# Kernel optimization log

Hardware: AMD Instinct MI355X
Metric: run time of the kernel (lower is better)

## Reference

```python
import jax, jax.numpy as jnp
import numpy as np


def conv2d(x, w, b, stride, pad):
    # x: NCHW, w: OIHW (torch layout)
    y = jax.lax.conv_general_dilated(
        x, w, (stride, stride), ((pad, pad), (pad, pad)),
        dimension_numbers=('NCHW', 'OIHW', 'NCHW'))
    return y + b[None, :, None, None]


def conv_transpose2d(x, w, b, stride, pad):
    # w: torch ConvTranspose2d layout [in, out, kH, kW]
    k = w.shape[2]
    w_t = jnp.flip(w, (2, 3)).transpose(1, 0, 2, 3)  # -> OIHW
    p = k - 1 - pad
    y = jax.lax.conv_general_dilated(
        x, w_t, (1, 1), ((p, p), (p, p)), lhs_dilation=(stride, stride),
        dimension_numbers=('NCHW', 'OIHW', 'NCHW'))
    return y + b[None, :, None, None]


def resblock(x, w1, b1, w2, b2):
    h = jax.nn.relu(x)
    h = conv2d(h, w1, b1, 1, 1)   # 3x3
    h = jax.nn.relu(h)
    h = conv2d(h, w2, b2, 1, 0)   # 1x1
    return x + h


def setup_inputs() -> dict:
    key = jax.random.key(0)
    ks = iter(jax.random.split(key, 32))
    K, D = 512, 256
    s = 0.05

    def rn(shape):
        return (jax.random.normal(next(ks), shape, dtype=jnp.float32) * s)

    inp = {
        'x': jax.random.uniform(next(ks), (32, 3, 128, 128), dtype=jnp.float32),
        'e_c1_w': rn((256, 3, 4, 4)),   'e_c1_b': jnp.zeros((256,), jnp.float32),
        'e_c2_w': rn((256, 256, 4, 4)), 'e_c2_b': jnp.zeros((256,), jnp.float32),
        'e_r1_w1': rn((256, 256, 3, 3)), 'e_r1_b1': jnp.zeros((256,), jnp.float32),
        'e_r1_w2': rn((256, 256, 1, 1)), 'e_r1_b2': jnp.zeros((256,), jnp.float32),
        'e_r2_w1': rn((256, 256, 3, 3)), 'e_r2_b1': jnp.zeros((256,), jnp.float32),
        'e_r2_w2': rn((256, 256, 1, 1)), 'e_r2_b2': jnp.zeros((256,), jnp.float32),
        'emb': jax.random.normal(next(ks), (K, D), dtype=jnp.float32) / K,
        'd_r1_w1': rn((256, 256, 3, 3)), 'd_r1_b1': jnp.zeros((256,), jnp.float32),
        'd_r1_w2': rn((256, 256, 1, 1)), 'd_r1_b2': jnp.zeros((256,), jnp.float32),
        'd_r2_w1': rn((256, 256, 3, 3)), 'd_r2_b1': jnp.zeros((256,), jnp.float32),
        'd_r2_w2': rn((256, 256, 1, 1)), 'd_r2_b2': jnp.zeros((256,), jnp.float32),
        'd_t1_w': rn((256, 256, 4, 4)), 'd_t1_b': jnp.zeros((256,), jnp.float32),
        'd_t2_w': rn((256, 3, 4, 4)),   'd_t2_b': jnp.zeros((3,), jnp.float32),
    }
    return inp


def reference(x, e_c1_w, e_c1_b, e_c2_w, e_c2_b,
              e_r1_w1, e_r1_b1, e_r1_w2, e_r1_b2,
              e_r2_w1, e_r2_b1, e_r2_w2, e_r2_b2,
              emb,
              d_r1_w1, d_r1_b1, d_r1_w2, d_r1_b2,
              d_r2_w1, d_r2_b1, d_r2_w2, d_r2_b2,
              d_t1_w, d_t1_b, d_t2_w, d_t2_b):
    # ---- encoder ----
    h = jax.nn.relu(conv2d(x, e_c1_w, e_c1_b, 2, 1))
    h = jax.nn.relu(conv2d(h, e_c2_w, e_c2_b, 2, 1))
    h = resblock(h, e_r1_w1, e_r1_b1, e_r1_w2, e_r1_b2)
    z_e_x = resblock(h, e_r2_w1, e_r2_b1, e_r2_w2, e_r2_b2)  # [B,256,h,w]

    # ---- VQ: fused squared-distance + argmin (same math as
    # sum((z - e)^2, -2).argmin(-1), without the (B,h,w,256,K) intermediate) ----
    z = z_e_x.transpose(0, 2, 3, 1)                      # [B,h,w,256]
    z2 = jnp.sum(z * z, axis=-1, keepdims=True)          # [B,h,w,1]
    e2 = jnp.sum(emb * emb, axis=-1)                     # [K]
    dists = z2 - 2.0 * jnp.einsum('bhwd,kd->bhwk', z, emb) + e2
    latents = jnp.argmin(dists, axis=-1)                 # [B,h,w] int

    # ---- decoder ----
    z_q = emb[latents]                                   # [B,h,w,256]
    z_q_x = z_q.transpose(0, 3, 1, 2)                    # [B,256,h,w]
    d = resblock(z_q_x, d_r1_w1, d_r1_b1, d_r1_w2, d_r1_b2)
    d = resblock(d, d_r2_w1, d_r2_b1, d_r2_w2, d_r2_b2)
    d = jax.nn.relu(conv_transpose2d(d, d_t1_w, d_t1_b, 2, 1))
    x_tilde = jax.nn.sigmoid(conv_transpose2d(d, d_t2_w, d_t2_b, 2, 1))
    return x_tilde, z_e_x, z_q_x
```

## Files before the change

### kernel.cpp

```cpp
#include <hip/hip_runtime.h>
#include <math.h>

using frag_ab = __attribute__((ext_vector_type(8))) short;
using f32x4   = __attribute__((ext_vector_type(4))) float;

__device__ __forceinline__ unsigned short f2b(float f) {
    unsigned u = __float_as_uint(f);
    u += 0x7fffu + ((u >> 16) & 1u);
    return (unsigned short)(u >> 16);
}
__device__ __forceinline__ void bf8_to_f(uint4 v, float* f) {
    const unsigned* p = (const unsigned*)&v;
    #pragma unroll
    for (int q = 0; q < 4; ++q) {
        unsigned u = p[q];
        f[2*q]   = __uint_as_float(u << 16);
        f[2*q+1] = __uint_as_float(u & 0xffff0000u);
    }
}
__device__ __forceinline__ void gload16(const void* g, void* l) {
    __builtin_amdgcn_global_load_lds(g, l, 16, 0, 0);
}

__global__ void k_wt(const float* __restrict__ in, unsigned short* __restrict__ out,
                     int total, int CO, int CI, int sO, int sI) {
    int i = blockIdx.x * 256 + threadIdx.x;
    if (i >= total) return;
    int ci = i % CI;
    int r  = i / CI;
    int co = r % CO;
    int tp = r / CO;
    out[i] = f2b(in[(size_t)co * sO + (size_t)ci * sI + tp]);
}
__global__ void k_wt16(const float* __restrict__ in, unsigned short* __restrict__ out,
                       int sO, int sI) {
    int i = blockIdx.x * 256 + threadIdx.x;
    int ci = i & 255, co = i >> 8;
    const float* p = in + (size_t)co * sO + (size_t)ci * sI;
    #pragma unroll
    for (int tp = 0; tp < 16; ++tp)
        out[tp * 65536 + i] = f2b(p[tp]);
}
__global__ void k_wt3(const float* p0, const float* p1, const float* p2, const float* p3,
                      unsigned short* o0, unsigned short* o1, unsigned short* o2,
                      unsigned short* o3) {
    int z = blockIdx.y;
    const float* in = (z == 0) ? p0 : (z == 1) ? p1 : (z == 2) ? p2 : p3;
    unsigned short* out = (z == 0) ? o0 : (z == 1) ? o1 : (z == 2) ? o2 : o3;
    int i = blockIdx.x * 256 + threadIdx.x;
    int ci = i & 255, co = i >> 8;
    const float* p = in + (size_t)co * 2304 + (size_t)ci * 9;
    #pragma unroll
    for (int tp = 0; tp < 9; ++tp)
        out[tp * 65536 + i] = f2b(p[tp]);
}
__global__ void k_wt1(const float* p0, const float* p1, const float* p2, const float* p3,
                      unsigned short* o0, unsigned short* o1, unsigned short* o2,
                      unsigned short* o3) {
    int z = blockIdx.y;
    const float* in = (z == 0) ? p0 : (z == 1) ? p1 : (z == 2) ? p2 : p3;
    unsigned short* out = (z == 0) ? o0 : (z == 1) ? o1 : (z == 2) ? o2 : o3;
    int i = blockIdx.x * 256 + threadIdx.x;
    int ci = i & 255, co = i >> 8;
    out[i] = f2b(in[co * 256 + ci]);
}
__global__ void k_embcast(const float* __restrict__ in, unsigned short* __restrict__ out) {
    int i = blockIdx.x * 256 + threadIdx.x;
    out[i] = f2b(in[i]);
}

__global__ void k_e2(const float* __restrict__ emb, float* __restrict__ e2,
                     float* __restrict__ zpad) {
    if (blockIdx.x == 2) { zpad[threadIdx.x] = 0.f; return; }
    int k = blockIdx.x * 256 + threadIdx.x;
    if (k < 512) {
        const float* r = emb + k * 256;
        float s = 0.f;
        #pragma unroll 8
        for (int d = 0; d < 256; ++d) s += r[d] * r[d];
        e2[k] = s;
    }
}

__global__ __launch_bounds__(256) void k_conv1(const float* __restrict__ x,
        const float* __restrict__ w, const float* __restrict__ bias,
        unsigned short* __restrict__ out) {
    int t = threadIdx.x;
    int y = blockIdx.x * 4 + (t >> 6);
    int xq = t & 63;
    int b = blockIdx.y;
    int co0 = blockIdx.z * 64;
    float patch[48];
    #pragma unroll
    for (int ci = 0; ci < 3; ++ci)
        #pragma unroll
        for (int ky = 0; ky < 4; ++ky)
            #pragma unroll
            for (int kx = 0; kx < 4; ++kx) {
                int sy = 2*y - 1 + ky, sx = 2*xq - 1 + kx;
                float v = 0.f;
                if ((unsigned)sy < 128u && (unsigned)sx < 128u)
                    v = x[((b*3 + ci)*128 + sy)*128 + sx];
                patch[(ci*4 + ky)*4 + kx] = v;
            }
    unsigned short* op = out + (((size_t)(b*64 + y)*64 + xq) << 8) + co0;
    for (int c8 = 0; c8 < 8; ++c8) {
        unsigned short u8[8];
        #pragma unroll
        for (int cc = 0; cc < 8; ++cc) {
            int co = co0 + c8*8 + cc;
            float a = bias[co];
            #pragma unroll
            for (int k = 0; k < 48; ++k) a = fmaf(w[co*48 + k], patch[k], a);
            u8[cc] = f2b(fmaxf(a, 0.f));
        }
        *(uint4*)(op + c8*8) = *(uint4*)u8;
    }
}

template<int MODE, bool RELU_OUT, bool RELU_B16>
__global__ __launch_bounds__(256) void k_cgemm(
        const unsigned short* __restrict__ A,
        const unsigned short* __restrict__ Wt,
        const float* __restrict__ bias,
        const float* __restrict__ skipF,
        const unsigned short* __restrict__ zpad,
        unsigned short* __restrict__ outB,
        float* __restrict__ outFn,
        float* __restrict__ outFc) {
    constexpr int NTAPS = (MODE==0) ? 16 : (MODE==1) ? 9 : (MODE==2) ? 1 : 4;
    constexpr int NCH   = NTAPS * 4;
    constexpr int HIN   = (MODE==0) ? 64 : 32;
    constexpr bool ISCT = (MODE==3);

    __shared__ __align__(16) unsigned short As[2][128*64];
    __shared__ __align__(16) unsigned short Bs[2][128*64];

    int t = threadIdx.x;
    int cob = blockIdx.x;
    int y0  = blockIdx.y * 4;
    int bz  = blockIdx.z;
    int b   = ISCT ? (bz >> 2) : bz;
    int par = ISCT ? (bz & 3) : 0;
    int psy = par >> 1, psx = par & 1;

    int srow = t >> 3;
    int scc  = t & 7;
    int sc2  = scc ^ (srow & 7);

    int wv = t >> 6, lane = t & 63;
    int mq = (wv >> 1) * 64, nq = (wv & 1) * 64;
    int lg = lane >> 4, lr = lane & 15;

    f32x4 acc[4][4];
    #pragma unroll
    for (int i = 0; i < 4; ++i)
        #pragma unroll
        for (int j = 0; j < 4; ++j) acc[i][j] = (f32x4){0.f,0.f,0.f,0.f};

    auto stage = [&](int n, int buf) {
        int tap = n >> 2, kk0 = (n & 3) * 64;
        int tdy, tdx, wtap;
        if (MODE == 0)      { tdy = tap >> 2; tdx = tap & 3; wtap = tap; }
        else if (MODE == 1) { tdy = tap / 3;  tdx = tap % 3; wtap = tap; }
        else if (MODE == 2) { tdy = 0; tdx = 0; wtap = 0; }
        else { int jy = tap >> 1, jx = tap & 1;
               tdy = psy - jy; tdx = psx - jx;
               wtap = ((psy ? 0 : 1) + 2*jy) * 4 + ((psx ? 0 : 1) + 2*jx); }
        const unsigned short* wb = Wt + ((size_t)wtap << 16) + ((size_t)cob << 15);
        #pragma unroll
        for (int q = 0; q < 4; ++q) {
            int row = srow + 32*q;
            int soy = y0 + (row >> 5), sox = row & 31;
            int sy = (MODE == 0) ? (2*soy - 1 + tdy)
                   : (MODE == 1) ? (soy - 1 + tdy) : (soy + tdy);
            int sx = (MODE == 0) ? (2*sox - 1 + tdx)
                   : (MODE == 1) ? (sox - 1 + tdx) : (sox + tdx);
            bool val = ((unsigned)sy < (unsigned)HIN) && ((unsigned)sx < (unsigned)HIN);
            const unsigned short* asrc = val
                ? A + ((((size_t)(b*HIN + sy))*HIN + sx) << 8) + kk0 + sc2*8
                : zpad;
            gload16(asrc, (char*)As[buf] + q*4096 + t*16);
            gload16(wb + (((size_t)row) << 8) + kk0 + sc2*8,
                    (char*)Bs[buf] + q*4096 + t*16);
        }
    };

    stage(0, 0);
    __syncthreads();
    for (int n = 0; n < NCH; ++n) {
        int cur = n & 1;
        if (n + 1 < NCH) stage(n + 1, cur ^ 1);
        #pragma unroll
        for (int ks = 0; ks < 2; ++ks) {
            int c = ks*4 + lg;
            frag_ab af[4], bf[4];
            #pragma unroll
            for (int i = 0; i < 4; ++i) {
                int ar = mq + i*16 + lr;
                af[i] = *(const frag_ab*)((const char*)As[cur] + ar*128 + ((c ^ (ar & 7)) << 4));
                int br = nq + i*16 + lr;
                bf[i] = *(const frag_ab*)((const char*)Bs[cur] + br*128 + ((c ^ (br & 7)) << 4));
            }
            #pragma unroll
            for (int i = 0; i < 4; ++i)
                #pragma unroll
                for (int j = 0; j < 4; ++j)
                    acc[i][j] = __builtin_amdgcn_mfma_f32_16x16x32_bf16(
                                    af[i], bf[j], acc[i][j], 0, 0, 0);
        }
        __syncthreads();
    }

    #pragma unroll
    for (int mf = 0; mf < 4; ++mf) {
        #pragma unroll
        for (int nf = 0; nf < 4; ++nf) {
            int co = cob*128 + nq + nf*16 + lr;
            float bb = bias[co];
            f32x4 v = acc[mf][nf];
            #pragma unroll
            for (int j = 0; j < 4; ++j) {
                int prow = mq + mf*16 + lg*4 + j;
                int oy = y0 + (prow >> 5);
                int ox = prow & 31;
                size_t pix;
                if (ISCT) pix = ((size_t)(b*64 + (2*oy + psy)))*64 + (2*ox + psx);
                else      pix = ((size_t)(b*32 + oy))*32 + ox;
                float xv = v[j] + bb;
                if (skipF) xv += skipF[pix*256 + co];
                if (RELU_OUT) xv = fmaxf(xv, 0.f);
                if (outB)  outB[pix*256 + co] = f2b(RELU_B16 ? fmaxf(xv, 0.f) : xv);
                if (outFn) outFn[pix*256 + co] = xv;
                if (outFc) outFc[(((size_t)b*256 + co) << 10) + oy*32 + ox] = xv;
            }
        }
    }
}

__global__ __launch_bounds__(256) void k_vqm(const unsigned short* __restrict__ zB,
        const unsigned short* __restrict__ eB,
        const float* __restrict__ e2, int* __restrict__ lat) {
    __shared__ __align__(16) unsigned short As[64*256];
    __shared__ __align__(16) unsigned short Bs[64*256];
    int t = threadIdx.x;
    int pos0 = blockIdx.x * 64;
    #pragma unroll
    for (int q = 0; q < 8; ++q) {
        int idx = q*256 + t;
        int row = idx >> 5, ch = idx & 31;
        uint4 v = *(const uint4*)(zB + (((size_t)(pos0 + row)) << 8) + ch*8);
        *(uint4*)((char*)As + row*512 + ((ch ^ (row & 7)) << 4)) = v;
    }
    int wv = t >> 6, lane = t & 63;
    int lg = lane >> 4, lr = lane & 15;
    int arow = wv*16 + lr;
    int aswz[8];
    #pragma unroll
    for (int kk = 0; kk < 8; ++kk)
        aswz[kk] = arow*512 + (((kk*4 + lg) ^ (arow & 7)) << 4);
    float minv[4] = {1e30f, 1e30f, 1e30f, 1e30f};
    int   mink[4] = {0, 0, 0, 0};
    for (int kc = 0; kc < 8; ++kc) {
        __syncthreads();
        #pragma unroll
        for (int q = 0; q < 8; ++q) {
            int idx = q*256 + t;
            int row = idx >> 5, ch = idx & 31;
            uint4 v = *(const uint4*)(eB + (((size_t)(kc*64 + row)) << 8) + ch*8);
            *(uint4*)((char*)Bs + row*512 + ((ch ^ (row & 7)) << 4)) = v;
        }
        __syncthreads();
        #pragma unroll
        for (int nt = 0; nt < 4; ++nt) {
            int brow = nt*16 + lr;
            f32x4 acc = (f32x4){0.f, 0.f, 0.f, 0.f};
            #pragma unroll
            for (int kk = 0; kk < 8; ++kk) {
                frag_ab a = *(const frag_ab*)((const char*)As + aswz[kk]);
                frag_ab b = *(const frag_ab*)((const char*)Bs
                              + brow*512 + (((kk*4 + lg) ^ (brow & 7)) << 4));
                acc = __builtin_amdgcn_mfma_f32_16x16x32_bf16(a, b, acc, 0, 0, 0);
            }
            int k = kc*64 + nt*16 + lr;
            float ee = e2[k];
            #pragma unroll
            for (int j = 0; j < 4; ++j) {
                float dist = ee - 2.f * acc[j];
                if (dist < minv[j]) { minv[j] = dist; mink[j] = k; }
            }
        }
    }
    #pragma unroll
    for (int s = 1; s < 16; s <<= 1) {
        #pragma unroll
        for (int j = 0; j < 4; ++j) {
            float ov = __shfl_xor(minv[j], s, 64);
            int   ok = __shfl_xor(mink[j], s, 64);
            if (ov < minv[j] || (ov == minv[j] && ok < mink[j])) {
                minv[j] = ov; mink[j] = ok;
            }
        }
    }
    if (lr == 0) {
        #pragma unroll
        for (int j = 0; j < 4; ++j)
            lat[pos0 + wv*16 + lg*4 + j] = mink[j];
    }
}

__global__ __launch_bounds__(256) void k_gather(const int* __restrict__ lat,
        const float* __restrict__ emb, float* __restrict__ zqc,
        unsigned short* __restrict__ zqB, float* __restrict__ zqF) {
    __shared__ int ll[32];
    int t = threadIdx.x, y = blockIdx.x, b = blockIdx.y;
    if (t < 32) ll[t] = lat[(b * 32 + y) * 32 + t];
    __syncthreads();
    #pragma unroll
    for (int i = 0; i < 32; ++i) {
        int l = i * 256 + t;
        int d = l >> 5, xx = l & 31;
        zqc[(((size_t)b*256 + d) << 10) + y*32 + xx] = emb[ll[xx]*256 + d];
    }
    int xx = t & 31, dg = t >> 5;
    const float* e = emb + ll[xx]*256 + dg*32;
    size_t off = ((((size_t)(b*32 + y)*32 + xx)) << 8) + dg*32;
    #pragma unroll
    for (int q = 0; q < 8; ++q) {
        float4 v = *(const float4*)(e + q*4);
        *(float4*)(zqF + off + q*4) = v;
        uint2 pk;
        pk.x = (unsigned)f2b(fmaxf(v.x, 0.f)) | ((unsigned)f2b(fmaxf(v.y, 0.f)) << 16);
        pk.y = (unsigned)f2b(fmaxf(v.z, 0.f)) | ((unsigned)f2b(fmaxf(v.w, 0.f)) << 16);
        *(uint2*)(zqB + off + q*4) = pk;
    }
}

__global__ __launch_bounds__(256) void k_convt2(const unsigned short* __restrict__ in,
        const unsigned short* __restrict__ Wt,
        const float* __restrict__ bias, float* __restrict__ out) {
    __shared__ __align__(16) unsigned short slab[4*66*40];
    __shared__ __align__(16) unsigned short wl[16*3*32];
    int t = threadIdx.x;
    int b = blockIdx.y;
    int oy0 = blockIdx.x * 4;
    int u0 = oy0 >> 1;
    int oyl = t >> 7, ox = t & 127;
    int sy = oyl & 1, sx = ox & 1;
    int v = ox >> 1;
    float acc0[3] = {0.f,0.f,0.f}, acc1[3] = {0.f,0.f,0.f};
    for (int kc = 0; kc < 8; ++kc) {
        __syncthreads();
        for (int i = t; i < 4*66*4; i += 256) {
            int g = i & 3; int cidx = i >> 2;
            int cc = cidx % 66, ri = cidx / 66;
            int iy = u0 - 1 + ri, ix = cc - 1;
            uint4 v4 = {0,0,0,0};
            if ((unsigned)iy < 64u && (unsigned)ix < 64u)
                v4 = *(const uint4*)(in + (((size_t)(b*64 + iy)*64 + ix) << 8)
                                        + kc*32 + g*8);
            *(uint4*)(&slab[(ri*66 + cc)*40 + g*8]) = v4;
        }
        for (int i = t; i < 1536; i += 256)
            wl[i] = Wt[(i >> 5) * 256 + kc*32 + (i & 31)];
        __syncthreads();
        #pragma unroll
        for (int jy = 0; jy < 2; ++jy) {
            int duy = sy - jy;
            int riA = 1 + duy;
            #pragma unroll
            for (int jx = 0; jx < 2; ++jx) {
                int dvx = sx - jx;
                int cc = v + dvx + 1;
                int wtap = ((sy ? 0 : 1) + 2*jy)*4 + ((sx ? 0 : 1) + 2*jx);
                const unsigned short* sA = &slab[(riA*66 + cc)*40];
                const unsigned short* sB = sA + 66*40;
                const unsigned short* wp = &wl[wtap*96];
                #pragma unroll
                for (int c8 = 0; c8 < 4; ++c8) {
                    float fA[8], fB[8], w0[8], w1[8], w2[8];
                    bf8_to_f(*(const uint4*)(sA + c8*8), fA);
                    bf8_to_f(*(const uint4*)(sB + c8*8), fB);
                    bf8_to_f(*(const uint4*)(wp + c8*8), w0);
                    bf8_to_f(*(const uint4*)(wp + 32 + c8*8), w1);
                    bf8_to_f(*(const uint4*)(wp + 64 + c8*8), w2);
                    #pragma unroll
                    for (int q = 0; q < 8; ++q) {
                        acc0[0] = fmaf(fA[q], w0[q], acc0[0]);
                        acc0[1] = fmaf(fA[q], w1[q], acc0[1]);
                        acc0[2] = fmaf(fA[q], w2[q], acc0[2]);
                        acc1[0] = fmaf(fB[q], w0[q], acc1[0]);
                        acc1[1] = fmaf(fB[q], w1[q], acc1[1]);
                        acc1[2] = fmaf(fB[q], w2[q], acc1[2]);
                    }
                }
            }
        }
    }
    #pragma unroll
    for (int co = 0; co < 3; ++co) {
        float b0 = acc0[co] + bias[co];
        float b1 = acc1[co] + bias[co];
        out[(((size_t)b*3 + co) << 14) + (oy0 + oyl)*128 + ox]     = 1.f/(1.f + __expf(-b0));
        out[(((size_t)b*3 + co) << 14) + (oy0 + oyl + 2)*128 + ox] = 1.f/(1.f + __expf(-b1));
    }
}

extern "C" void kernel_launch(void* const* d_in, const int* in_sizes, int n_in,
                              void* d_out, int out_size, void* d_ws, size_t ws_size,
                              hipStream_t stream) {
    const float* x     = (const float*)d_in[0];
    const float* ec1w  = (const float*)d_in[1];
    const float* ec1b  = (const float*)d_in[2];
    const float* ec2w  = (const float*)d_in[3];
    const float* ec2b  = (const float*)d_in[4];
    const float* er1w1 = (const float*)d_in[5];
    const float* er1b1 = (const float*)d_in[6];
    const float* er1w2 = (const float*)d_in[7];
    const float* er1b2 = (const float*)d_in[8];
    const float* er2w1 = (const float*)d_in[9];
    const float* er2b1 = (const float*)d_in[10];
    const float* er2w2 = (const float*)d_in[11];
    const float* er2b2 = (const float*)d_in[12];
    const float* emb   = (const float*)d_in[13];
    const float* dr1w1 = (const float*)d_in[14];
    const float* dr1b1 = (const float*)d_in[15];
    const float* dr1w2 = (const float*)d_in[16];
    const float* dr1b2 = (const float*)d_in[17];
    const float* dr2w1 = (const float*)d_in[18];
    const float* dr2b1 = (const float*)d_in[19];
    const float* dr2w2 = (const float*)d_in[20];
    const float* dr2b2 = (const float*)d_in[21];
    const float* dt1w  = (const float*)d_in[22];
    const float* dt1b  = (const float*)d_in[23];
    const float* dt2w  = (const float*)d_in[24];
    const float* dt2b  = (const float*)d_in[25];

    float* outp = (float*)d_out;
    float* xt = outp;
    float* ze = outp + 1572864;
    float* zq = ze + 8388608;

    char* ws = (char*)d_ws;
    unsigned short* h1B  = (unsigned short*)(ws);
    unsigned short* B0   = (unsigned short*)(ws + 67108864);
    unsigned short* B1   = (unsigned short*)(ws + 83886080);
    unsigned short* T3   = (unsigned short*)(ws + 100663296);
    float*          F0   = (float*)(ws + 117440512);
    float*          F1   = (float*)(ws + 150994944);
    unsigned short* WtC2 = (unsigned short*)(ws + 184549376);
    unsigned short* Wt31 = (unsigned short*)(ws + 186646528);
    unsigned short* Wt32 = (unsigned short*)(ws + 187826176);
    unsigned short* Wt33 = (unsigned short*)(ws + 189005824);
    unsigned short* Wt34 = (unsigned short*)(ws + 190185472);
    unsigned short* W11  = (unsigned short*)(ws + 191365120);
    unsigned short* W12  = (unsigned short*)(ws + 191496192);
    unsigned short* W13  = (unsigned short*)(ws + 191627264);
    unsigned short* W14  = (unsigned short*)(ws + 191758336);
    unsigned short* WtT1 = (unsigned short*)(ws + 191889408);
    unsigned short* WtT2 = (unsigned short*)(ws + 193986560);
    float*          e2v  = (float*)(ws + 194011136);
    int*            lat  = (int*)(ws + 194013184);
    unsigned short* embB = (unsigned short*)(ws + 194144256);
    float*          zpad = (float*)(ws + 194406400);

    k_e2<<<3, 256, 0, stream>>>(emb, e2v, zpad);
    k_embcast<<<512, 256, 0, stream>>>(emb, embB);
    k_wt16<<<256, 256, 0, stream>>>(ec2w, WtC2, 4096, 16);
    k_wt16<<<256, 256, 0, stream>>>(dt1w, WtT1, 16, 4096);
    k_wt3<<<dim3(256, 4), 256, 0, stream>>>(er1w1, er2w1, dr1w1, dr2w1,
                                            Wt31, Wt32, Wt33, Wt34);
    k_wt1<<<dim3(256, 4), 256, 0, stream>>>(er1w2, er2w2, dr1w2, dr2w2,
                                            W11, W12, W13, W14);
    k_wt<<<48, 256, 0, stream>>>(dt2w, WtT2, 12288, 3, 256, 16, 48);

    const unsigned short* zp16 = (const unsigned short*)zpad;
    k_conv1<<<dim3(16, 32, 4), 256, 0, stream>>>(x, ec1w, ec1b, h1B);
    k_cgemm<0,true,false><<<dim3(2,8,32), 256, 0, stream>>>(h1B, WtC2, ec2b,
            nullptr, zp16, B0, F0, nullptr);
    k_cgemm<1,true,false><<<dim3(2,8,32), 256, 0, stream>>>(B0, Wt31, er1b1,
            nullptr, zp16, T3, nullptr, nullptr);
    k_cgemm<2,false,true><<<dim3(2,8,32), 256, 0, stream>>>(T3, W11, er1b2,
            F0, zp16, B1, F1, nullptr);
    k_cgemm<1,true,false><<<dim3(2,8,32), 256, 0, stream>>>(B1, Wt32, er2b1,
            nullptr, zp16, T3, nullptr, nullptr);
    k_cgemm<2,false,false><<<dim3(2,8,32), 256, 0, stream>>>(T3, W12, er2b2,
            F1, zp16, B0, nullptr, ze);
    k_vqm<<<512, 256, 0, stream>>>(B0, embB, e2v, lat);
    k_gather<<<dim3(32,32), 256, 0, stream>>>(lat, emb, zq, B0, F0);
    k_cgemm<1,true,false><<<dim3(2,8,32), 256, 0, stream>>>(B0, Wt33, dr1b1,
            nullptr, zp16, T3, nullptr, nullptr);
    k_cgemm<2,false,true><<<dim3(2,8,32), 256, 0, stream>>>(T3, W13, dr1b2,
            F0, zp16, B1, F1, nullptr);
    k_cgemm<1,true,false><<<dim3(2,8,32), 256, 0, stream>>>(B1, Wt34, dr2b1,
            nullptr, zp16, T3, nullptr, nullptr);
    k_cgemm<2,false,false><<<dim3(2,8,32), 256, 0, stream>>>(T3, W14, dr2b2,
            F1, zp16, B0, nullptr, nullptr);
    k_cgemm<3,true,false><<<dim3(2,8,128), 256, 0, stream>>>(B0, WtT1, dt1b,
            nullptr, zp16, h1B, nullptr, nullptr);
    k_convt2<<<dim3(32,32), 256, 0, stream>>>(h1B, WtT2, dt2b, xt);
}
```

Before: 964.6 us.

## Triple-buffer conv GEMM with 256x128 tiles, 512 threads, and LDS-staged conv1 weights

Result: slower. 1.080 ms (+12.0%).

```diff
diff --git a/kernel.cpp b/kernel.cpp
--- a/kernel.cpp
+++ b/kernel.cpp
@@ -85,11 +85,18 @@
 __global__ __launch_bounds__(256) void k_conv1(const float* __restrict__ x,
         const float* __restrict__ w, const float* __restrict__ bias,
         unsigned short* __restrict__ out) {
+    __shared__ float wl[64 * 49];
     int t = threadIdx.x;
-    int y = blockIdx.x * 4 + (t >> 6);
-    int xq = t & 63;
     int b = blockIdx.y;
     int co0 = blockIdx.z * 64;
+    for (int i = t; i < 3072; i += 256) {
+        int cl = i / 48, k = i % 48;
+        wl[cl * 49 + k] = w[(co0 + cl) * 48 + k];
+    }
+    __syncthreads();
+    int pxl = t >> 3, cch = t & 7;
+    int p = blockIdx.x * 32 + pxl;
+    int oy = p >> 6, ox = p & 63;
     float patch[48];
     #pragma unroll
     for (int ci = 0; ci < 3; ++ci)
@@ -97,29 +104,28 @@
         for (int ky = 0; ky < 4; ++ky)
             #pragma unroll
             for (int kx = 0; kx < 4; ++kx) {
-                int sy = 2*y - 1 + ky, sx = 2*xq - 1 + kx;
+                int sy = 2*oy - 1 + ky, sx = 2*ox - 1 + kx;
                 float v = 0.f;
                 if ((unsigned)sy < 128u && (unsigned)sx < 128u)
                     v = x[((b*3 + ci)*128 + sy)*128 + sx];
                 patch[(ci*4 + ky)*4 + kx] = v;
             }
-    unsigned short* op = out + (((size_t)(b*64 + y)*64 + xq) << 8) + co0;
-    for (int c8 = 0; c8 < 8; ++c8) {
-        unsigned short u8[8];
-        #pragma unroll
-        for (int cc = 0; cc < 8; ++cc) {
-            int co = co0 + c8*8 + cc;
-            float a = bias[co];
-            #pragma unroll
-            for (int k = 0; k < 48; ++k) a = fmaf(w[co*48 + k], patch[k], a);
-            u8[cc] = f2b(fmaxf(a, 0.f));
-        }
-        *(uint4*)(op + c8*8) = *(uint4*)u8;
-    }
+    unsigned short u8[8];
+    #pragma unroll
+    for (int cc = 0; cc < 8; ++cc) {
+        int cl = cch*8 + cc;
+        float a = bias[co0 + cl];
+        const float* wp = &wl[cl * 49];
+        #pragma unroll
+        for (int k = 0; k < 48; ++k) a = fmaf(wp[k], patch[k], a);
+        u8[cc] = f2b(fmaxf(a, 0.f));
+    }
+    size_t pix = (size_t)b * 4096 + p;
+    *(uint4*)(out + (pix << 8) + co0 + cch*8) = *(uint4*)u8;
 }
 
 template<int MODE, bool RELU_OUT, bool RELU_B16>
-__global__ __launch_bounds__(256) void k_cgemm(
+__global__ __launch_bounds__(512) void k_cgemm(
         const unsigned short* __restrict__ A,
         const unsigned short* __restrict__ Wt,
         const float* __restrict__ bias,
@@ -133,12 +139,12 @@
     constexpr int HIN   = (MODE==0) ? 64 : 32;
     constexpr bool ISCT = (MODE==3);
 
-    __shared__ __align__(16) unsigned short As[2][128*64];
-    __shared__ __align__(16) unsigned short Bs[2][128*64];
+    __shared__ __align__(16) unsigned short As[3][256*64];
+    __shared__ __align__(16) unsigned short Bs[3][128*64];
 
     int t = threadIdx.x;
     int cob = blockIdx.x;
-    int y0  = blockIdx.y * 4;
+    int y0  = blockIdx.y * 8;
     int bz  = blockIdx.z;
     int b   = ISCT ? (bz >> 2) : bz;
     int par = ISCT ? (bz & 3) : 0;
@@ -168,9 +174,11 @@
                tdy = psy - jy; tdx = psx - jx;
                wtap = ((psy ? 0 : 1) + 2*jy) * 4 + ((psx ? 0 : 1) + 2*jx); }
         const unsigned short* wb = Wt + ((size_t)wtap << 16) + ((size_t)cob << 15);
+        char* Ad = (char*)As + buf * 32768;
+        char* Bd = (char*)Bs + buf * 16384;
         #pragma unroll
         for (int q = 0; q < 4; ++q) {
-            int row = srow + 32*q;
+            int row = srow + 64*q;
             int soy = y0 + (row >> 5), sox = row & 31;
             int sy = (MODE == 0) ? (2*soy - 1 + tdy)
                    : (MODE == 1) ? (soy - 1 + tdy) : (soy + tdy);
@@ -180,17 +188,18 @@
             const unsigned short* asrc = val
                 ? A + ((((size_t)(b*HIN + sy))*HIN + sx) << 8) + kk0 + sc2*8
                 : zpad;
-            gload16(asrc, (char*)As[buf] + q*4096 + t*16);
-            gload16(wb + (((size_t)row) << 8) + kk0 + sc2*8,
-                    (char*)Bs[buf] + q*4096 + t*16);
+            gload16(asrc, Ad + q*8192 + t*16);
+        }
+        #pragma unroll
+        for (int q = 0; q < 2; ++q) {
+            int row = srow + 64*q;
+            gload16(wb + (((size_t)row) << 8) + kk0 + sc2*8, Bd + q*8192 + t*16);
         }
     };
 
-    stage(0, 0);
-    __syncthreads();
-    for (int n = 0; n < NCH; ++n) {
-        int cur = n & 1;
-        if (n + 1 < NCH) stage(n + 1, cur ^ 1);
+    auto compute = [&](int buf) {
+        const char* Ab = (const char*)As + buf * 32768;
+        const char* Bb = (const char*)Bs + buf * 16384;
         #pragma unroll
         for (int ks = 0; ks < 2; ++ks) {
             int c = ks*4 + lg;
@@ -198,9 +207,9 @@
             #pragma unroll
             for (int i = 0; i < 4; ++i) {
                 int ar = mq + i*16 + lr;
-                af[i] = *(const frag_ab*)((const char*)As[cur] + ar*128 + ((c ^ (ar & 7)) << 4));
+                af[i] = *(const frag_ab*)(Ab + ar*128 + ((c ^ (ar & 7)) << 4));
                 int br = nq + i*16 + lr;
-                bf[i] = *(const frag_ab*)((const char*)Bs[cur] + br*128 + ((c ^ (br & 7)) << 4));
+                bf[i] = *(const frag_ab*)(Bb + br*128 + ((c ^ (br & 7)) << 4));
             }
             #pragma unroll
             for (int i = 0; i < 4; ++i)
@@ -209,7 +218,25 @@
                     acc[i][j] = __builtin_amdgcn_mfma_f32_16x16x32_bf16(
                                     af[i], bf[j], acc[i][j], 0, 0, 0);
         }
-        __syncthreads();
+    };
+
+    stage(0, 0);
+    stage(1, 1);
+    int cur = 0;
+    for (int n = 0; n < NCH; ++n) {
+        if (n + 2 < NCH) {
+            int pre = cur + 2; if (pre >= 3) pre -= 3;
+            stage(n + 2, pre);
+            asm volatile("s_waitcnt vmcnt(12)" ::: "memory");
+        } else if (n + 1 < NCH) {
+            asm volatile("s_waitcnt vmcnt(6)" ::: "memory");
+        } else {
+            asm volatile("s_waitcnt vmcnt(0)" ::: "memory");
+        }
+        __builtin_amdgcn_s_barrier();
+        compute(cur);
+        __builtin_amdgcn_s_barrier();
+        cur = (cur == 2) ? 0 : cur + 1;
     }
 
     #pragma unroll
@@ -475,28 +502,28 @@
     k_wt<<<48, 256, 0, stream>>>(dt2w, WtT2, 12288, 3, 256, 16, 48);
 
     const unsigned short* zp16 = (const unsigned short*)zpad;
-    k_conv1<<<dim3(16, 32, 4), 256, 0, stream>>>(x, ec1w, ec1b, h1B);
-    k_cgemm<0,true,false><<<dim3(2,8,32), 256, 0, stream>>>(h1B, WtC2, ec2b,
+    k_conv1<<<dim3(128, 32, 4), 256, 0, stream>>>(x, ec1w, ec1b, h1B);
+    k_cgemm<0,true,false><<<dim3(2,4,32), 512, 0, stream>>>(h1B, WtC2, ec2b,
             nullptr, zp16, B0, F0, nullptr);
-    k_cgemm<1,true,false><<<dim3(2,8,32), 256, 0, stream>>>(B0, Wt31, er1b1,
+    k_cgemm<1,true,false><<<dim3(2,4,32), 512, 0, stream>>>(B0, Wt31, er1b1,
             nullptr, zp16, T3, nullptr, nullptr);
-    k_cgemm<2,false,true><<<dim3(2,8,32), 256, 0, stream>>>(T3, W11, er1b2,
+    k_cgemm<2,false,true><<<dim3(2,4,32), 512, 0, stream>>>(T3, W11, er1b2,
             F0, zp16, B1, F1, nullptr);
-    k_cgemm<1,true,false><<<dim3(2,8,32), 256, 0, stream>>>(B1, Wt32, er2b1,
+    k_cgemm<1,true,false><<<dim3(2,4,32), 512, 0, stream>>>(B1, Wt32, er2b1,
             nullptr, zp16, T3, nullptr, nullptr);
-    k_cgemm<2,false,false><<<dim3(2,8,32), 256, 0, stream>>>(T3, W12, er2b2,
+    k_cgemm<2,false,false><<<dim3(2,4,32), 512, 0, stream>>>(T3, W12, er2b2,
             F1, zp16, B0, nullptr, ze);
     k_vqm<<<512, 256, 0, stream>>>(B0, embB, e2v, lat);
     k_gather<<<dim3(32,32), 256, 0, stream>>>(lat, emb, zq, B0, F0);
-    k_cgemm<1,true,false><<<dim3(2,8,32), 256, 0, stream>>>(B0, Wt33, dr1b1,
+    k_cgemm<1,true,false><<<dim3(2,4,32), 512, 0, stream>>>(B0, Wt33, dr1b1,
             nullptr, zp16, T3, nullptr, nullptr);
-    k_cgemm<2,false,true><<<dim3(2,8,32), 256, 0, stream>>>(T3, W13, dr1b2,
+    k_cgemm<2,false,true><<<dim3(2,4,32), 512, 0, stream>>>(T3, W13, dr1b2,
             F0, zp16, B1, F1, nullptr);
-    k_cgemm<1,true,false><<<dim3(2,8,32), 256, 0, stream>>>(B1, Wt34, dr2b1,
+    k_cgemm<1,true,false><<<dim3(2,4,32), 512, 0, stream>>>(B1, Wt34, dr2b1,
             nullptr, zp16, T3, nullptr, nullptr);
-    k_cgemm<2,false,false><<<dim3(2,8,32), 256, 0, stream>>>(T3, W14, dr2b2,
+    k_cgemm<2,false,false><<<dim3(2,4,32), 512, 0, stream>>>(T3, W14, dr2b2,
             F1, zp16, B0, nullptr, nullptr);
-    k_cgemm<3,true,false><<<dim3(2,8,128), 256, 0, stream>>>(B0, WtT1, dt1b,
+    k_cgemm<3,true,false><<<dim3(2,4,128), 512, 0, stream>>>(B0, WtT1, dt1b,
             nullptr, zp16, h1B, nullptr, nullptr);
     k_convt2<<<dim3(32,32), 256, 0, stream>>>(h1B, WtT2, dt2b, xt);
 }
```
